# Kernel tuning notes

Hardware: AMD Instinct MI355X
Metric: run time of the kernel (lower is better)

## Reference

```python
import jax, jax.numpy as jnp
import numpy as np

B, C, H, W = 1024, 256, 16, 16  # must satisfy H*W == C per the module's bmm(v, attn)


def setup_inputs() -> dict:
    key = jax.random.key(0)
    ks = jax.random.split(key, 8)
    s = 1.0 / np.sqrt(C)
    return {
        "x": jax.random.normal(ks[0], (B, C, H, W), dtype=jnp.float32),
        "Wq": jax.random.normal(ks[1], (C, C), dtype=jnp.float32) * s,
        "bq": jax.random.normal(ks[2], (C,), dtype=jnp.float32) * s,
        "Wk": jax.random.normal(ks[3], (C, C), dtype=jnp.float32) * s,
        "bk": jax.random.normal(ks[4], (C,), dtype=jnp.float32) * s,
        "Wv": jax.random.normal(ks[5], (C, C), dtype=jnp.float32) * s,
        "bv": jax.random.normal(ks[6], (C,), dtype=jnp.float32) * s,
        "gamma": jax.random.normal(ks[7], (1,), dtype=jnp.float32),
    }


def reference(x, Wq, bq, Wk, bk, Wv, bv, gamma):
    b, c, h, w = x.shape
    n = h * w  # equals c by construction

    def conv1x1(Wt, bt):
        # 1x1 conv == per-pixel channel GEMM
        return jnp.einsum('oi,bihw->bohw', Wt, x) + bt[None, :, None, None]

    q = conv1x1(Wq, bq).reshape(b, c, n)            # (B, C, N)
    k = conv1x1(Wk, bk).reshape(b, c, n)            # (B, C, N)
    v = conv1x1(Wv, bv).reshape(b, c, n)            # (B, C, N)

    # attn = bmm(q, k^T) / sqrt(C) -> (B, C, C); softmax over last dim
    scale = jnp.asarray(1.0 / np.sqrt(c), dtype=x.dtype)
    attn = jax.nn.softmax(jnp.einsum('bcn,bdn->bcd', q, k) * scale, axis=-1)

    # out = bmm(v, attn): (B, C, N=C) @ (B, C, C) -> (B, C, C), reshape to (B,C,H,W)
    out = jnp.einsum('bcn,bnd->bcd', v, attn).reshape(b, c, h, w)
    return gamma * out + x
```

## Files before the change

kernel.cpp:

```cpp
#include <hip/hip_runtime.h>


typedef __attribute__((ext_vector_type(8))) short bf16x8;
typedef __attribute__((ext_vector_type(4))) short bf16x4;
typedef __attribute__((ext_vector_type(4))) float f32x4;

#define MFMA16(a, b, c) __builtin_amdgcn_mfma_f32_16x16x32_bf16((a), (b), (c), 0, 0, 0)

#define GLDS16(g, l)                                                      \
  __builtin_amdgcn_global_load_lds(                                       \
      (const __attribute__((address_space(1))) void*)(g),                 \
      (__attribute__((address_space(3))) void*)(l), 16, 0, 0)

static __device__ __forceinline__ unsigned short f2bf(float f) {
  unsigned int u = __float_as_uint(f);
  u += 0x7fffu + ((u >> 16) & 1u);
  return (unsigned short)(u >> 16);
}

static __device__ __forceinline__ int swz(int row, int byteInRow) {
  return row * 512 + (byteInRow ^ ((row & 7) << 4));
}

__global__ void k_prep(const float* __restrict__ Wq, const float* __restrict__ bq,
                       const float* __restrict__ Wk, const float* __restrict__ bk,
                       const float* __restrict__ Wv, const float* __restrict__ bv,
                       const float* __restrict__ gamma,
                       unsigned short* __restrict__ W3h, float* __restrict__ b3) {
  const int r = blockIdx.x;
  const int p = r >> 8, sr = r & 255;
  const float s = (p == 0) ? 0.0625f : (p == 1 ? 1.0f : gamma[0]);
  const float* W = (p == 0) ? Wq : (p == 1 ? Wk : Wv);
  const float* bs = (p == 0) ? bq : (p == 1 ? bk : bv);
  W3h[r * 256 + threadIdx.x] = f2bf(W[sr * 256 + threadIdx.x] * s);
  if (threadIdx.x == 0) b3[r] = bs[sr] * s;
}

__global__ __launch_bounds__(256, 3) void k_gemm2(
    const unsigned short* __restrict__ W3h, const float* __restrict__ b3,
    const float* __restrict__ x, unsigned short* __restrict__ Y) {
  __shared__ char smem[50176];
  float* TS = (float*)(smem + 32768);
  const int bid = blockIdx.x;
  const int swzb = (bid & 7) * 1536 + (bid >> 3);
  const int r_t = swzb % 6, bn_t = swzb / 6;
  const int m0 = r_t * 128, n0 = bn_t * 128;
  const int bb = n0 >> 8, nl0 = n0 & 255;
  const float* xb = x + (size_t)bb * 65536;
  const int tid = threadIdx.x, wv = tid >> 6, lane = tid & 63;
  const int lo = lane & 15, hi = lane >> 4;
  const int wm = wv >> 1, wn = wv & 1;
  const int tr = tid >> 4, tc = (tid & 15) * 4;

  f32x4 acc[4][4];
#pragma unroll
  for (int i = 0; i < 4; ++i)
#pragma unroll
    for (int j = 0; j < 4; ++j) acc[i][j] = (f32x4){0.f, 0.f, 0.f, 0.f};

  for (int k0 = 0; k0 < 256; k0 += 64) {
#pragma unroll
    for (int j = 0; j < 4; ++j) {
      const int s = j * 256 + tid;
      const int row = s >> 3, gs = (s & 7) ^ (row & 7);
      GLDS16(W3h + (size_t)(m0 + row) * 256 + k0 + gs * 8,
             smem + j * 4096 + wv * 1024);
    }

#pragma unroll
    for (int c = 0; c < 2; ++c) {
      if (c == 1) __syncthreads();
#pragma unroll
      for (int j = 0; j < 4; ++j) {
        float4 xg = *(const float4*)(xb + (k0 + tr + j * 16) * 256 + nl0 + c * 64 + tc);
        *(float4*)(&TS[(tr + j * 16) * 68 + tc]) = xg;
      }
      __syncthreads();
#pragma unroll
      for (int ff = 0; ff < 2; ++ff) {
        const int g = wv + ff * 4;
        const int n = lane;
        bf16x8 v;
#pragma unroll
        for (int j = 0; j < 8; ++j) v[j] = (short)f2bf(TS[(g * 8 + j) * 68 + n]);
        const int row = c * 64 + n;
        *(bf16x8*)(smem + 16384 + row * 128 + ((g ^ (row & 7)) * 16)) = v;
      }
    }
    __syncthreads();

#pragma unroll
    for (int kk = 0; kk < 2; ++kk) {
      bf16x8 a[4], b[4];
#pragma unroll
      for (int rt = 0; rt < 4; ++rt) {
        const int row = wm * 64 + rt * 16 + lo, g = kk * 4 + hi;
        a[rt] = *(const bf16x8*)(smem + row * 128 + ((g ^ (row & 7)) * 16));
      }
#pragma unroll
      for (int ct = 0; ct < 4; ++ct) {
        const int row = wn * 64 + ct * 16 + lo, g = kk * 4 + hi;
        b[ct] = *(const bf16x8*)(smem + 16384 + row * 128 + ((g ^ (row & 7)) * 16));
      }
#pragma unroll
      for (int rt = 0; rt < 4; ++rt)
#pragma unroll
        for (int ct = 0; ct < 4; ++ct) acc[rt][ct] = MFMA16(a[rt], b[ct], acc[rt][ct]);
    }
    __syncthreads();
  }

  float b3v[4][4];
#pragma unroll
  for (int rt = 0; rt < 4; ++rt)
#pragma unroll
    for (int reg = 0; reg < 4; ++reg)
      b3v[rt][reg] = b3[m0 + wm * 64 + rt * 16 + hi * 4 + reg];
#pragma unroll
  for (int rt = 0; rt < 4; ++rt)
#pragma unroll
    for (int ct = 0; ct < 4; ++ct)
#pragma unroll
      for (int reg = 0; reg < 4; ++reg) {
        const int m = wm * 64 + rt * 16 + hi * 4 + reg;
        const int n = wn * 64 + ct * 16 + lo;
        *(unsigned short*)(smem + m * 256 + ((n * 2) ^ ((m & 7) << 4))) =
            f2bf(acc[rt][ct][reg] + b3v[rt][reg]);
      }
  __syncthreads();
  const int p = m0 >> 8, sr0 = m0 & 255;
  unsigned short* dstb = Y + (size_t)bb * 196608 + (size_t)p * 65536;
#pragma unroll
  for (int j = 0; j < 8; ++j) {
    const int s = j * 256 + tid;
    const int m = s >> 4, pp = s & 15;
    const int ng = pp ^ (m & 7);
    int4 v = *(const int4*)(smem + m * 256 + pp * 16);
    *(int4*)(dstb + (size_t)(sr0 + m) * 256 + nl0 + ng * 8) = v;
  }
}

__global__ __launch_bounds__(512, 2) void attn5(
    const float* __restrict__ x, const unsigned short* __restrict__ Y,
    float* __restrict__ out) {
  __shared__ char smem[131072];
  const int b = blockIdx.x;
  const float* xb = x + (size_t)b * 65536;
  const unsigned short* Qb = Y + (size_t)b * 196608;
  const unsigned short* Kb = Qb + 65536;
  const unsigned short* Vb = Qb + 131072;
  const int tid = threadIdx.x, w = tid >> 6, lane = tid & 63;
  const int lo = lane & 15, hi = lane >> 4;
  const int r0 = w * 32;
  const int rb0 = (w >> 1) * 64, d0 = (w & 1) * 128;

#pragma unroll
  for (int i = 0; i < 16; ++i) {
    const int idx = i * 512 + tid;
    const int row = idx >> 5, c16 = idx & 31;
    const int gs = (c16 & 24) | ((c16 ^ row) & 7);
    GLDS16(Kb + (size_t)row * 256 + gs * 8, smem + idx * 16);
  }
  bf16x8 aq[2][8];
#pragma unroll
  for (int k0 = 0; k0 < 8; ++k0)
#pragma unroll
    for (int rt = 0; rt < 2; ++rt)
      aq[rt][k0] =
          *(const bf16x8*)(Qb + (size_t)(r0 + rt * 16 + lo) * 256 + k0 * 32 + hi * 8);
  __syncthreads();

  bf16x8 av[4][4];

  {
    f32x4 acc[2][16];
#pragma unroll
    for (int i = 0; i < 2; ++i)
#pragma unroll
      for (int j = 0; j < 16; ++j) acc[i][j] = (f32x4){0.f, 0.f, 0.f, 0.f};
#pragma unroll
    for (int k0 = 0; k0 < 8; ++k0)
#pragma unroll
      for (int ct = 0; ct < 16; ++ct) {
        bf16x8 bb = *(const bf16x8*)(smem + swz(ct * 16 + lo, (k0 * 32 + hi * 8) * 2));
        acc[0][ct] = MFMA16(aq[0][k0], bb, acc[0][ct]);
        acc[1][ct] = MFMA16(aq[1][k0], bb, acc[1][ct]);
      }
#pragma unroll
    for (int kq = 0; kq < 4; ++kq)
#pragma unroll
      for (int rt = 0; rt < 4; ++rt)
        av[rt][kq] =
            *(const bf16x8*)(Vb + (size_t)(rb0 + rt * 16 + lo) * 256 + kq * 32 + hi * 8);
#pragma unroll
    for (int rt = 0; rt < 2; ++rt)
#pragma unroll
      for (int reg = 0; reg < 4; ++reg) {
        float s = 0.f;
        float vals[16];
#pragma unroll
        for (int ct = 0; ct < 16; ++ct) {
          const float p = __expf(acc[rt][ct][reg]);
          vals[ct] = p;
          s += p;
        }
        s += __shfl_xor(s, 1);
        s += __shfl_xor(s, 2);
        s += __shfl_xor(s, 4);
        s += __shfl_xor(s, 8);
        const float inv = 1.0f / s;
#pragma unroll
        for (int ct = 0; ct < 16; ++ct) acc[rt][ct][reg] = vals[ct] * inv;
      }
    __syncthreads();
#pragma unroll
    for (int rt = 0; rt < 2; ++rt)
#pragma unroll
      for (int ct = 0; ct < 16; ++ct) {
        const int d = ct * 16 + lo;
        const int s0 = r0 + rt * 16 + hi * 4;
        bf16x4 v;
#pragma unroll
        for (int reg = 0; reg < 4; ++reg) v[reg] = (short)f2bf(acc[rt][ct][reg]);
        *(bf16x4*)(smem + swz(d, s0 * 2)) = v;
      }
  }
  __syncthreads();

  {
    f32x4 acc[4][8];
#pragma unroll
    for (int i = 0; i < 4; ++i)
#pragma unroll
      for (int j = 0; j < 8; ++j) acc[i][j] = (f32x4){0.f, 0.f, 0.f, 0.f};
#pragma unroll
    for (int k0 = 0; k0 < 4; ++k0)
#pragma unroll
      for (int ct = 0; ct < 8; ++ct) {
        bf16x8 bb = *(const bf16x8*)(smem + swz(d0 + ct * 16 + lo, (k0 * 32 + hi * 8) * 2));
#pragma unroll
        for (int rt = 0; rt < 4; ++rt) acc[rt][ct] = MFMA16(av[rt][k0], bb, acc[rt][ct]);
      }
#pragma unroll
    for (int k0 = 4; k0 < 8; ++k0) {
      bf16x8 a[4];
#pragma unroll
      for (int rt = 0; rt < 4; ++rt)
        a[rt] = *(const bf16x8*)(Vb + (size_t)(rb0 + rt * 16 + lo) * 256 + k0 * 32 + hi * 8);
#pragma unroll
      for (int ct = 0; ct < 8; ++ct) {
        bf16x8 bb = *(const bf16x8*)(smem + swz(d0 + ct * 16 + lo, (k0 * 32 + hi * 8) * 2));
#pragma unroll
        for (int rt = 0; rt < 4; ++rt) acc[rt][ct] = MFMA16(a[rt], bb, acc[rt][ct]);
      }
    }
    float* ob = out + (size_t)b * 65536;
#pragma unroll
    for (int rt = 0; rt < 4; ++rt)
#pragma unroll
      for (int reg = 0; reg < 4; ++reg) {
        const int c = rb0 + rt * 16 + hi * 4 + reg;
#pragma unroll
        for (int ct = 0; ct < 8; ++ct) {
          const int d = d0 + ct * 16 + lo;
          const int idx = c * 256 + d;
          ob[idx] = acc[rt][ct][reg] + xb[idx];
        }
      }
  }
}

extern "C" void kernel_launch(void* const* d_in, const int* in_sizes, int n_in,
                              void* d_out, int out_size, void* d_ws, size_t ws_size,
                              hipStream_t stream) {
  const float* x = (const float*)d_in[0];
  const float* Wq = (const float*)d_in[1];
  const float* bq = (const float*)d_in[2];
  const float* Wk = (const float*)d_in[3];
  const float* bk = (const float*)d_in[4];
  const float* Wv = (const float*)d_in[5];
  const float* bv = (const float*)d_in[6];
  const float* gamma = (const float*)d_in[7];
  float* out = (float*)d_out;

  unsigned short* Y = (unsigned short*)d_ws;
  unsigned short* W3h = Y + (size_t)1024 * 196608;
  float* b3 = (float*)(W3h + 768 * 256);
  const size_t need = ((size_t)1024 * 196608 + 768 * 256) * 2 + 768 * 4;
  if (ws_size < need) return;

  hipLaunchKernelGGL(k_prep, dim3(768), dim3(256), 0, stream,
                     Wq, bq, Wk, bk, Wv, bv, gamma, W3h, b3);
  hipLaunchKernelGGL(k_gemm2, dim3(12288), dim3(256), 0, stream, W3h, b3, x, Y);
  hipLaunchKernelGGL(attn5, dim3(1024), dim3(512), 0, stream, x, Y, out);
}
```

Measured before the change: 508.9 us.

## Enlarge QKV projection GEMM tile to 256x128 and stage x via async LDS loads

Result: slower. 519.9 us (+2.2%).

```diff
diff --git a/kernel.cpp b/kernel.cpp
--- a/kernel.cpp
+++ b/kernel.cpp
@@ -36,21 +36,20 @@
   if (threadIdx.x == 0) b3[r] = bs[sr] * s;
 }
 
-__global__ __launch_bounds__(256, 3) void k_gemm2(
+__global__ __launch_bounds__(512, 4) void k_gemm3(
     const unsigned short* __restrict__ W3h, const float* __restrict__ b3,
     const float* __restrict__ x, unsigned short* __restrict__ Y) {
-  __shared__ char smem[50176];
-  float* TS = (float*)(smem + 32768);
+  __shared__ char smem[81920];
   const int bid = blockIdx.x;
-  const int swzb = (bid & 7) * 1536 + (bid >> 3);
-  const int r_t = swzb % 6, bn_t = swzb / 6;
-  const int m0 = r_t * 128, n0 = bn_t * 128;
+  const int swzb = (bid & 7) * 768 + (bid >> 3);
+  const int r_t = swzb % 3, bn_t = swzb / 3;
+  const int m0 = r_t * 256, n0 = bn_t * 128;
   const int bb = n0 >> 8, nl0 = n0 & 255;
   const float* xb = x + (size_t)bb * 65536;
   const int tid = threadIdx.x, wv = tid >> 6, lane = tid & 63;
   const int lo = lane & 15, hi = lane >> 4;
   const int wm = wv >> 1, wn = wv & 1;
-  const int tr = tid >> 4, tc = (tid & 15) * 4;
+  float* TSf = (float*)(smem + 49152);
 
   f32x4 acc[4][4];
 #pragma unroll
@@ -61,51 +60,49 @@
   for (int k0 = 0; k0 < 256; k0 += 64) {
 #pragma unroll
     for (int j = 0; j < 4; ++j) {
-      const int s = j * 256 + tid;
-      const int row = s >> 3, gs = (s & 7) ^ (row & 7);
-      GLDS16(W3h + (size_t)(m0 + row) * 256 + k0 + gs * 8,
-             smem + j * 4096 + wv * 1024);
-    }
-
-#pragma unroll
-    for (int c = 0; c < 2; ++c) {
-      if (c == 1) __syncthreads();
-#pragma unroll
-      for (int j = 0; j < 4; ++j) {
-        float4 xg = *(const float4*)(xb + (k0 + tr + j * 16) * 256 + nl0 + c * 64 + tc);
-        *(float4*)(&TS[(tr + j * 16) * 68 + tc]) = xg;
-      }
-      __syncthreads();
-#pragma unroll
-      for (int ff = 0; ff < 2; ++ff) {
-        const int g = wv + ff * 4;
-        const int n = lane;
-        bf16x8 v;
-#pragma unroll
-        for (int j = 0; j < 8; ++j) v[j] = (short)f2bf(TS[(g * 8 + j) * 68 + n]);
-        const int row = c * 64 + n;
-        *(bf16x8*)(smem + 16384 + row * 128 + ((g ^ (row & 7)) * 16)) = v;
-      }
+      const int s = j * 512 + tid;
+      const int row = s >> 3, g = s & 7;
+      const int gs = g ^ (row & 7);
+      GLDS16(W3h + (size_t)(m0 + row) * 256 + k0 + gs * 8, smem + s * 16);
+    }
+#pragma unroll
+    for (int j = 0; j < 4; ++j) {
+      const int s = j * 512 + tid;
+      const int row = s >> 5, g4 = s & 31;
+      GLDS16(xb + (size_t)(k0 + row) * 256 + nl0 + g4 * 4,
+             smem + 49152 + s * 16);
+    }
+    __syncthreads();
+
+#pragma unroll
+    for (int ff = 0; ff < 2; ++ff) {
+      const int slot = ff * 512 + tid;
+      const int n = slot & 127, g = slot >> 7;
+      bf16x8 v;
+#pragma unroll
+      for (int j = 0; j < 8; ++j) v[j] = (short)f2bf(TSf[(g * 8 + j) * 128 + n]);
+      *(bf16x8*)(smem + 32768 + n * 128 + ((g ^ (n & 7)) * 16)) = v;
     }
     __syncthreads();
 
 #pragma unroll
     for (int kk = 0; kk < 2; ++kk) {
-      bf16x8 a[4], b[4];
+      bf16x8 a[4], bfr[4];
+      const int g = kk * 4 + hi;
 #pragma unroll
       for (int rt = 0; rt < 4; ++rt) {
-        const int row = wm * 64 + rt * 16 + lo, g = kk * 4 + hi;
+        const int row = wm * 64 + rt * 16 + lo;
         a[rt] = *(const bf16x8*)(smem + row * 128 + ((g ^ (row & 7)) * 16));
       }
 #pragma unroll
       for (int ct = 0; ct < 4; ++ct) {
-        const int row = wn * 64 + ct * 16 + lo, g = kk * 4 + hi;
-        b[ct] = *(const bf16x8*)(smem + 16384 + row * 128 + ((g ^ (row & 7)) * 16));
+        const int row = wn * 64 + ct * 16 + lo;
+        bfr[ct] = *(const bf16x8*)(smem + 32768 + row * 128 + ((g ^ (row & 7)) * 16));
       }
 #pragma unroll
       for (int rt = 0; rt < 4; ++rt)
 #pragma unroll
-        for (int ct = 0; ct < 4; ++ct) acc[rt][ct] = MFMA16(a[rt], b[ct], acc[rt][ct]);
+        for (int ct = 0; ct < 4; ++ct) acc[rt][ct] = MFMA16(a[rt], bfr[ct], acc[rt][ct]);
     }
     __syncthreads();
   }
@@ -128,15 +125,14 @@
             f2bf(acc[rt][ct][reg] + b3v[rt][reg]);
       }
   __syncthreads();
-  const int p = m0 >> 8, sr0 = m0 & 255;
-  unsigned short* dstb = Y + (size_t)bb * 196608 + (size_t)p * 65536;
+  unsigned short* dstb = Y + (size_t)bb * 196608 + (size_t)r_t * 65536;
 #pragma unroll
   for (int j = 0; j < 8; ++j) {
-    const int s = j * 256 + tid;
+    const int s = j * 512 + tid;
     const int m = s >> 4, pp = s & 15;
     const int ng = pp ^ (m & 7);
     int4 v = *(const int4*)(smem + m * 256 + pp * 16);
-    *(int4*)(dstb + (size_t)(sr0 + m) * 256 + nl0 + ng * 8) = v;
+    *(int4*)(dstb + (size_t)m * 256 + nl0 + ng * 8) = v;
   }
 }
 
@@ -291,6 +287,6 @@
 
   hipLaunchKernelGGL(k_prep, dim3(768), dim3(256), 0, stream,
                      Wq, bq, Wk, bk, Wv, bv, gamma, W3h, b3);
-  hipLaunchKernelGGL(k_gemm2, dim3(12288), dim3(256), 0, stream, W3h, b3, x, Y);
+  hipLaunchKernelGGL(k_gemm3, dim3(6144), dim3(512), 0, stream, W3h, b3, x, Y);
   hipLaunchKernelGGL(attn5, dim3(1024), dim3(512), 0, stream, x, Y, out);
 }
```
